# Kernel tuning notes

Hardware: AMD Instinct MI355X
Metric: run time of the kernel (lower is better)

## Reference

```python
import jax, jax.numpy as jnp
import numpy as np

N_DATA = 128      # number of datasets (process conditions)
SEG_LEN = 131072  # thickness points per dataset
N_MAT = 8         # number of distinct materials
N_MATP = 8        # material params: Sigma0, BetaD, Ea, Mfda, Di, A0, B0, l0
N_PROCP = 5       # process params: SigmaC, K0, alpha1, L0, GrainSize_200
RGAS = 8.314      # gas constant, J/(mol K)


def setup_inputs() -> dict:
    key = jax.random.key(0)
    k1, k2, k3, k4 = jax.random.split(key, 4)
    # thickness points: sorted within each dataset segment, scaled to [0, 1]
    x = jax.random.uniform(k1, (N_DATA, SEG_LEN), dtype=jnp.float32)
    x_scaled = jnp.sort(x, axis=1).reshape(-1)
    # process conditions [R, T, P, Melting_T]
    pc = jax.random.uniform(k2, (N_DATA, 4), dtype=jnp.float32)
    R = 0.05 + pc[:, 0]            # deposition rate
    T = 300.0 + 300.0 * pc[:, 1]   # temperature (K)
    P = 0.1 + pc[:, 2]             # pressure
    material_index = jnp.sort(jax.random.randint(k3, (N_DATA,), 0, N_MAT, dtype=jnp.int32))
    melting_T = 1000.0 + 100.0 * material_index.astype(jnp.float32)
    process_c = jnp.stack([R, T, P, melting_T], axis=1)
    # learned raw parameters (pre-sigmoid) and bounds
    n_params = N_MAT * N_MATP + N_DATA * N_PROCP  # 704
    raw_params = 0.5 * jax.random.normal(k4, (n_params,), dtype=jnp.float32)
    para_lb = jnp.full((n_params,), 0.1, dtype=jnp.float32)
    para_ub = jnp.full((n_params,), 2.0, dtype=jnp.float32)
    # MinMaxScaler surrogates: [x_data_min, x_data_max, y_data_min, y_data_max], feature_range=(0,1)
    scaler_params = jnp.array([0.5, 500.0, -50.0, 50.0], dtype=jnp.float32)
    fit_index = jnp.repeat(jnp.arange(1, N_DATA + 1, dtype=jnp.int32), SEG_LEN)
    return {
        'x_scaled': x_scaled, 'process_c': process_c, 'raw_params': raw_params,
        'para_lb': para_lb, 'para_ub': para_ub, 'scaler_params': scaler_params,
        'fit_index': fit_index, 'material_index': material_index,
    }


def _stress(tp, R, T, P, SigmaC, alpha1, L0, G200, Sigma0, BetaD, Ea, Mfda, Di, A0, B0, l0):
    """Kinetic stress equation (Chason-type). tp: [N, L-1]; params broadcast [N, 1]."""
    Lg = G200 * (tp / 200.0 + 1e-3) ** alpha1 + L0      # grain size evolution
    D = Di * jnp.exp(-Ea / (RGAS * T))                   # thermally activated diffusivity
    beta = BetaD * D / (R * Lg + 1e-9)                   # kinetic competition factor
    sigma_ss = (SigmaC - Mfda * P + (Sigma0 / Lg) * beta) / (1.0 + beta)
    return sigma_ss + A0 * jnp.exp(-tp / (B0 * l0 + 1e-9))  # steady-state + transient


def reference(x_scaled, process_c, raw_params, para_lb, para_ub, scaler_params,
              fit_index, material_index):
    n_data = process_c.shape[0]
    seg = x_scaled.shape[0] // n_data
    # unscale parameters: sigmoid -> [lb, ub]
    xv = jax.nn.sigmoid(raw_params) * (para_ub - para_lb) + para_lb
    materials = xv[:N_MAT * N_MATP].reshape(N_MAT, N_MATP)
    process = xv[N_MAT * N_MATP:].reshape(n_data, N_PROCP)
    x_min, x_max, y_min, y_max = scaler_params[0], scaler_params[1], scaler_params[2], scaler_params[3]
    # inverse MinMax transform of thickness (feature_range = (0, 1))
    t = (x_scaled * (x_max - x_min) + x_min).reshape(n_data, seg)  # [N, L]
    SigmaC, K0, alpha1, L0, G200 = (process[:, i:i + 1] for i in range(5))
    mat = materials[material_index]  # [N, 8] gather per-dataset material params
    Sigma0, BetaD, Ea, Mfda, Di, A0, B0, l0 = (mat[:, i:i + 1] for i in range(8))
    R, T, P = process_c[:, 0:1], process_c[:, 1:2], process_c[:, 2:3]
    # Euler integration: Fit[j+1] = Fit[j] + stress(t[j]) * dT  ==  K0 + cumsum
    s = _stress(t[:, :-1], R, T, P, SigmaC, alpha1, L0, G200,
                Sigma0, BetaD, Ea, Mfda, Di, A0, B0, l0)   # [N, L-1]
    dT = jnp.diff(t, axis=1)                                # [N, L-1]
    fit = jnp.concatenate([K0, K0 + jnp.cumsum(s * dT, axis=1)], axis=1).reshape(-1)
    # forward MinMax transform of stress-thickness (feature_range = (0, 1))
    return (fit - y_min) / (y_max - y_min)
```

## Files before the change

### kernel.cpp

```cpp
#include <hip/hip_runtime.h>

#define N_DATA   128
#define SEG_LEN  131072
#define NPROD    (SEG_LEN - 1)
#define N_MAT    8
#define N_MATP   8
#define N_PROCP  5
#define RGAS     8.314f

#define NCH      64
#define CHUNK    2048
#define TPB      256
#define EPT      8
#define NBLK     (N_DATA * NCH)

typedef float nt4 __attribute__((ext_vector_type(4)));

__device__ __forceinline__ float stress_s(float t,
    float alpha1, float L0, float G200, float Sigma0, float A0,
    float inv_tau, float cbd, float base_num, float R) {
  float Lg  = G200 * __expf(alpha1 * __logf(t * (1.0f / 200.0f) + 0.001f)) + L0;
  float u   = R * Lg + 1e-9f;
  float num = base_num * u * Lg + Sigma0 * cbd;
  float den = Lg * (u + cbd);
  float sigma_ss = num * __builtin_amdgcn_rcpf(den);
  return sigma_ss + A0 * __expf(-t * inv_tau);
}

__global__ __launch_bounds__(TPB) void k0_init(unsigned long long* __restrict__ cs) {
  cs[blockIdx.x * TPB + threadIdx.x] = 0ull;
}

__global__ __launch_bounds__(TPB) void k_scan(
    const float* __restrict__ x,
    const float* __restrict__ pc, const float* __restrict__ raw,
    const float* __restrict__ lb, const float* __restrict__ ub,
    const float* __restrict__ sc, const int* __restrict__ mat_idx,
    unsigned long long* __restrict__ cs,
    float* __restrict__ out) {
  __shared__ float pv[13];
  __shared__ float wtot[4];
  __shared__ float choff_s;

  int b   = blockIdx.x;
  int row = b >> 6;
  int ch  = b & (NCH - 1);
  int tid = threadIdx.x;
  int lane = tid & 63, wv = tid >> 6;

  long rowbase = (long)row * SEG_LEN;
  int  gb = ch * CHUNK + tid * EPT;
  const float* xp = x + rowbase + gb;
  float4 a  = *(const float4*)xp;
  float4 bq = *(const float4*)(xp + 4);
  float  xn = (gb + EPT < SEG_LEN) ? xp[EPT] : 0.0f;

  if (tid < 13) {
    int idx = (tid < 5) ? (N_MAT * N_MATP + row * N_PROCP + tid)
                        : (mat_idx[row] * N_MATP + (tid - 5));
    float s = 1.0f / (1.0f + __expf(-raw[idx]));
    pv[tid] = s * (ub[idx] - lb[idx]) + lb[idx];
  }
  __syncthreads();

  float SigmaC = pv[0], K0 = pv[1], alpha1 = pv[2], L0 = pv[3], G200 = pv[4];
  float Sigma0 = pv[5], BetaD = pv[6], Ea = pv[7], Mfda = pv[8], Di = pv[9];
  float A0 = pv[10], B0 = pv[11], l0 = pv[12];
  float R = pc[row * 4 + 0], T = pc[row * 4 + 1], P = pc[row * 4 + 2];
  float cbd      = BetaD * Di * __expf(-Ea / (RGAS * T));
  float base_num = SigmaC - Mfda * P;
  float inv_tau  = 1.0f / (B0 * l0 + 1e-9f);
  float x_min = sc[0], x_sc = sc[1] - sc[0];
  float y_min = sc[2], inv_yr = 1.0f / (sc[3] - sc[2]);

  float tv[9];
  tv[0] = a.x  * x_sc + x_min; tv[1] = a.y  * x_sc + x_min;
  tv[2] = a.z  * x_sc + x_min; tv[3] = a.w  * x_sc + x_min;
  tv[4] = bq.x * x_sc + x_min; tv[5] = bq.y * x_sc + x_min;
  tv[6] = bq.z * x_sc + x_min; tv[7] = bq.w * x_sc + x_min;
  tv[8] = xn   * x_sc + x_min;

  float pref[EPT];
  float run = 0.0f;
#pragma unroll
  for (int k = 0; k < EPT; k++) {
    float p = 0.0f;
    if (gb + k < NPROD) {
      float s = stress_s(tv[k], alpha1, L0, G200, Sigma0, A0, inv_tau, cbd, base_num, R);
      p = s * (tv[k + 1] - tv[k]);
    }
    run += p;
    pref[k] = run;
  }

  float incl = run;
#pragma unroll
  for (int d = 1; d < 64; d <<= 1) {
    float n = __shfl_up(incl, d);
    if (lane >= d) incl += n;
  }
  if (lane == 63) wtot[wv] = incl;
  __syncthreads();

  if (tid == 0) {
    float tot = wtot[0] + wtot[1] + wtot[2] + wtot[3];
    unsigned long long u = (1ull << 32) |
        (unsigned long long)__float_as_uint(tot);
    __hip_atomic_store(cs + b, u, __ATOMIC_RELAXED, __HIP_MEMORY_SCOPE_AGENT);
  }

  if (tid < 64) {
    float v = 0.0f;
    int l = tid;
    if (l < ch) {
      const unsigned long long* p = cs + ((row << 6) | l);
      unsigned long long u;
      do {
        u = __hip_atomic_load(p, __ATOMIC_RELAXED, __HIP_MEMORY_SCOPE_AGENT);
      } while ((u >> 32) == 0ull);
      v = __uint_as_float((unsigned)u);
    }
#pragma unroll
    for (int d = 32; d > 0; d >>= 1) v += __shfl_down(v, d);
    if (tid == 0) choff_s = v;
  }
  __syncthreads();

  float choff = choff_s;
  float low = 0.0f;
#pragma unroll
  for (int w = 0; w < 4; w++) low += (w < wv) ? wtot[w] : 0.0f;

  float base = K0 + choff + (incl - run) + low;
  nt4 o0, o1;
  o0.x = (base           - y_min) * inv_yr;
  o0.y = (base + pref[0] - y_min) * inv_yr;
  o0.z = (base + pref[1] - y_min) * inv_yr;
  o0.w = (base + pref[2] - y_min) * inv_yr;
  o1.x = (base + pref[3] - y_min) * inv_yr;
  o1.y = (base + pref[4] - y_min) * inv_yr;
  o1.z = (base + pref[5] - y_min) * inv_yr;
  o1.w = (base + pref[6] - y_min) * inv_yr;
  nt4* op = (nt4*)(out + rowbase + gb);
  __builtin_nontemporal_store(o0, op);
  __builtin_nontemporal_store(o1, op + 1);
}

extern "C" void kernel_launch(void* const* d_in, const int* in_sizes, int n_in,
                              void* d_out, int out_size, void* d_ws, size_t ws_size,
                              hipStream_t stream) {
  const float* x_scaled  = (const float*)d_in[0];
  const float* process_c = (const float*)d_in[1];
  const float* raw       = (const float*)d_in[2];
  const float* lb        = (const float*)d_in[3];
  const float* ub        = (const float*)d_in[4];
  const float* sc        = (const float*)d_in[5];
  const int*   mat_idx   = (const int*)d_in[7];
  float* out = (float*)d_out;
  unsigned long long* cs = (unsigned long long*)d_ws;

  k0_init<<<NBLK / TPB, TPB, 0, stream>>>(cs);
  k_scan<<<NBLK, TPB, 0, stream>>>(
      x_scaled, process_c, raw, lb, ub, sc, mat_idx, cs, out);
}
```

Before: 189.3 us.

## Make each wavefront an independent scan unit, dropping block-level shared memory and barriers

Each 64-lane wavefront now scans its own chunk of 1024 elements, 16 per thread instead of 8, and publishes its total to the global flag array on its own. Because no lane depends on other waves in the block, the shared-memory staging and __syncthreads barriers go away, and parameters are spread across lanes with shuffles. The cost is twice as many partial sums per row (128 instead of 64), so each wave's lookback may now loop over more flags. Higher register use per thread could also lower occupancy.

```diff
diff --git a/kernel.cpp b/kernel.cpp
--- a/kernel.cpp
+++ b/kernel.cpp
@@ -8,11 +8,12 @@
 #define N_PROCP  5
 #define RGAS     8.314f
 
-#define NCH      64
-#define CHUNK    2048
 #define TPB      256
-#define EPT      8
-#define NBLK     (N_DATA * NCH)
+#define EPT      16
+#define WCHUNK   (64 * EPT)
+#define WPR      (SEG_LEN / WCHUNK)
+#define NWAVE    (N_DATA * WPR)
+#define NBLK     (NWAVE / (TPB / 64))
 
 typedef float nt4 __attribute__((ext_vector_type(4)));
 
@@ -38,34 +39,34 @@
     const float* __restrict__ sc, const int* __restrict__ mat_idx,
     unsigned long long* __restrict__ cs,
     float* __restrict__ out) {
-  __shared__ float pv[13];
-  __shared__ float wtot[4];
-  __shared__ float choff_s;
-
-  int b   = blockIdx.x;
-  int row = b >> 6;
-  int ch  = b & (NCH - 1);
-  int tid = threadIdx.x;
-  int lane = tid & 63, wv = tid >> 6;
+  int tid  = threadIdx.x;
+  int lane = tid & 63;
+  int w    = blockIdx.x * (TPB >> 6) + (tid >> 6);
+  int row  = __builtin_amdgcn_readfirstlane(w >> 7);
+  int s    = w & (WPR - 1);
 
   long rowbase = (long)row * SEG_LEN;
-  int  gb = ch * CHUNK + tid * EPT;
-  const float* xp = x + rowbase + gb;
-  float4 a  = *(const float4*)xp;
-  float4 bq = *(const float4*)(xp + 4);
-  float  xn = (gb + EPT < SEG_LEN) ? xp[EPT] : 0.0f;
+  int  gbl = s * WCHUNK + lane * EPT;
+  const float* xp = x + rowbase + gbl;
+  float4 a0 = *(const float4*)(xp);
+  float4 a1 = *(const float4*)(xp + 4);
+  float4 a2 = *(const float4*)(xp + 8);
+  float4 a3 = *(const float4*)(xp + 12);
+  float  xn = (gbl + EPT < SEG_LEN) ? xp[EPT] : 0.0f;
 
-  if (tid < 13) {
-    int idx = (tid < 5) ? (N_MAT * N_MATP + row * N_PROCP + tid)
-                        : (mat_idx[row] * N_MATP + (tid - 5));
-    float s = 1.0f / (1.0f + __expf(-raw[idx]));
-    pv[tid] = s * (ub[idx] - lb[idx]) + lb[idx];
+  float pvl = 0.0f;
+  if (lane < 13) {
+    int idx = (lane < 5) ? (N_MAT * N_MATP + row * N_PROCP + lane)
+                         : (mat_idx[row] * N_MATP + (lane - 5));
+    float sg = 1.0f / (1.0f + __expf(-raw[idx]));
+    pvl = sg * (ub[idx] - lb[idx]) + lb[idx];
   }
-  __syncthreads();
+  float SigmaC = __shfl(pvl, 0),  K0   = __shfl(pvl, 1), alpha1 = __shfl(pvl, 2);
+  float L0     = __shfl(pvl, 3),  G200 = __shfl(pvl, 4);
+  float Sigma0 = __shfl(pvl, 5),  BetaD = __shfl(pvl, 6), Ea = __shfl(pvl, 7);
+  float Mfda   = __shfl(pvl, 8),  Di   = __shfl(pvl, 9);
+  float A0     = __shfl(pvl, 10), B0   = __shfl(pvl, 11), l0 = __shfl(pvl, 12);
 
-  float SigmaC = pv[0], K0 = pv[1], alpha1 = pv[2], L0 = pv[3], G200 = pv[4];
-  float Sigma0 = pv[5], BetaD = pv[6], Ea = pv[7], Mfda = pv[8], Di = pv[9];
-  float A0 = pv[10], B0 = pv[11], l0 = pv[12];
   float R = pc[row * 4 + 0], T = pc[row * 4 + 1], P = pc[row * 4 + 2];
   float cbd      = BetaD * Di * __expf(-Ea / (RGAS * T));
   float base_num = SigmaC - Mfda * P;
@@ -73,24 +74,27 @@
   float x_min = sc[0], x_sc = sc[1] - sc[0];
   float y_min = sc[2], inv_yr = 1.0f / (sc[3] - sc[2]);
 
-  float tv[9];
-  tv[0] = a.x  * x_sc + x_min; tv[1] = a.y  * x_sc + x_min;
-  tv[2] = a.z  * x_sc + x_min; tv[3] = a.w  * x_sc + x_min;
-  tv[4] = bq.x * x_sc + x_min; tv[5] = bq.y * x_sc + x_min;
-  tv[6] = bq.z * x_sc + x_min; tv[7] = bq.w * x_sc + x_min;
-  tv[8] = xn   * x_sc + x_min;
+  float xr[EPT + 1];
+  xr[0]=a0.x; xr[1]=a0.y; xr[2]=a0.z; xr[3]=a0.w;
+  xr[4]=a1.x; xr[5]=a1.y; xr[6]=a1.z; xr[7]=a1.w;
+  xr[8]=a2.x; xr[9]=a2.y; xr[10]=a2.z; xr[11]=a2.w;
+  xr[12]=a3.x; xr[13]=a3.y; xr[14]=a3.z; xr[15]=a3.w;
+  xr[16]=xn;
 
   float pref[EPT];
-  float run = 0.0f;
+  float run  = 0.0f;
+  float tcur = xr[0] * x_sc + x_min;
 #pragma unroll
   for (int k = 0; k < EPT; k++) {
+    float tnext = xr[k + 1] * x_sc + x_min;
     float p = 0.0f;
-    if (gb + k < NPROD) {
-      float s = stress_s(tv[k], alpha1, L0, G200, Sigma0, A0, inv_tau, cbd, base_num, R);
-      p = s * (tv[k + 1] - tv[k]);
+    if (gbl + k < NPROD) {
+      float ss = stress_s(tcur, alpha1, L0, G200, Sigma0, A0, inv_tau, cbd, base_num, R);
+      p = ss * (tnext - tcur);
     }
     run += p;
     pref[k] = run;
+    tcur = tnext;
   }
 
   float incl = run;
@@ -99,51 +103,49 @@
     float n = __shfl_up(incl, d);
     if (lane >= d) incl += n;
   }
-  if (lane == 63) wtot[wv] = incl;
-  __syncthreads();
 
-  if (tid == 0) {
-    float tot = wtot[0] + wtot[1] + wtot[2] + wtot[3];
+  if (lane == 63) {
     unsigned long long u = (1ull << 32) |
-        (unsigned long long)__float_as_uint(tot);
-    __hip_atomic_store(cs + b, u, __ATOMIC_RELAXED, __HIP_MEMORY_SCOPE_AGENT);
+        (unsigned long long)__float_as_uint(incl);
+    __hip_atomic_store(cs + w, u, __ATOMIC_RELAXED, __HIP_MEMORY_SCOPE_AGENT);
   }
 
-  if (tid < 64) {
-    float v = 0.0f;
-    int l = tid;
-    if (l < ch) {
-      const unsigned long long* p = cs + ((row << 6) | l);
-      unsigned long long u;
-      do {
-        u = __hip_atomic_load(p, __ATOMIC_RELAXED, __HIP_MEMORY_SCOPE_AGENT);
-      } while ((u >> 32) == 0ull);
-      v = __uint_as_float((unsigned)u);
-    }
+  float v = 0.0f;
+  for (int c = lane; c < s; c += 64) {
+    const unsigned long long* p = cs + ((row << 7) + c);
+    unsigned long long u;
+    do {
+      u = __hip_atomic_load(p, __ATOMIC_RELAXED, __HIP_MEMORY_SCOPE_AGENT);
+    } while (!(unsigned)(u >> 32));
+    v += __uint_as_float((unsigned)u);
+  }
 #pragma unroll
-    for (int d = 32; d > 0; d >>= 1) v += __shfl_down(v, d);
-    if (tid == 0) choff_s = v;
-  }
-  __syncthreads();
+  for (int d = 32; d > 0; d >>= 1) v += __shfl_down(v, d);
+  float choff = __shfl(v, 0);
 
-  float choff = choff_s;
-  float low = 0.0f;
-#pragma unroll
-  for (int w = 0; w < 4; w++) low += (w < wv) ? wtot[w] : 0.0f;
-
-  float base = K0 + choff + (incl - run) + low;
-  nt4 o0, o1;
-  o0.x = (base           - y_min) * inv_yr;
-  o0.y = (base + pref[0] - y_min) * inv_yr;
-  o0.z = (base + pref[1] - y_min) * inv_yr;
-  o0.w = (base + pref[2] - y_min) * inv_yr;
-  o1.x = (base + pref[3] - y_min) * inv_yr;
-  o1.y = (base + pref[4] - y_min) * inv_yr;
-  o1.z = (base + pref[5] - y_min) * inv_yr;
-  o1.w = (base + pref[6] - y_min) * inv_yr;
-  nt4* op = (nt4*)(out + rowbase + gb);
+  float base = K0 + choff + (incl - run);
+  nt4 o0, o1, o2, o3;
+  o0.x = (base            - y_min) * inv_yr;
+  o0.y = (base + pref[0]  - y_min) * inv_yr;
+  o0.z = (base + pref[1]  - y_min) * inv_yr;
+  o0.w = (base + pref[2]  - y_min) * inv_yr;
+  o1.x = (base + pref[3]  - y_min) * inv_yr;
+  o1.y = (base + pref[4]  - y_min) * inv_yr;
+  o1.z = (base + pref[5]  - y_min) * inv_yr;
+  o1.w = (base + pref[6]  - y_min) * inv_yr;
+  o2.x = (base + pref[7]  - y_min) * inv_yr;
+  o2.y = (base + pref[8]  - y_min) * inv_yr;
+  o2.z = (base + pref[9]  - y_min) * inv_yr;
+  o2.w = (base + pref[10] - y_min) * inv_yr;
+  o3.x = (base + pref[11] - y_min) * inv_yr;
+  o3.y = (base + pref[12] - y_min) * inv_yr;
+  o3.z = (base + pref[13] - y_min) * inv_yr;
+  o3.w = (base + pref[14] - y_min) * inv_yr;
+  nt4* op = (nt4*)(out + rowbase + gbl);
   __builtin_nontemporal_store(o0, op);
   __builtin_nontemporal_store(o1, op + 1);
+  __builtin_nontemporal_store(o2, op + 2);
+  __builtin_nontemporal_store(o3, op + 3);
 }
 
 extern "C" void kernel_launch(void* const* d_in, const int* in_sizes, int n_in,
@@ -159,7 +161,7 @@
   float* out = (float*)d_out;
   unsigned long long* cs = (unsigned long long*)d_ws;
 
-  k0_init<<<NBLK / TPB, TPB, 0, stream>>>(cs);
+  k0_init<<<NWAVE / TPB, TPB, 0, stream>>>(cs);
   k_scan<<<NBLK, TPB, 0, stream>>>(
       x_scaled, process_c, raw, lb, ub, sc, mat_idx, cs, out);
 }
```

Measured after the change: 203.1 us. 7.3% more time.
